# Performance work log

Measured on AMD Instinct MI355X. Metric: run time of the kernel, lower is better.

The kernel has to match this reference:

```python
import jax, jax.numpy as jnp
import numpy as np

TAU = 0.1
EPS = 1e-8

def _l2norm(x, axis):
    # matches F.normalize: x / max(||x||, 1e-12)
    n = jnp.sqrt(jnp.sum(x * x, axis=axis, keepdims=True))
    return x / jnp.maximum(n, 1e-12)

def setup_inputs() -> dict:
    key = jax.random.key(0)
    k1, k2, k3 = jax.random.split(key, 3)
    B, D, K = 262144, 256, 64
    return {
        "features": jax.random.normal(k1, (B, D), dtype=jnp.float32),
        "prototypes": jax.random.normal(k2, (K, D), dtype=jnp.float32),
        "domain_labels": jax.random.randint(k3, (B,), 0, K, dtype=jnp.int64),
    }

def reference(features, prototypes, domain_labels):
    f = _l2norm(features, 1)            # (B, D)
    p = _l2norm(prototypes, 1)          # (K, D)
    sim = jnp.einsum('bd,kd->bk', f, p) / TAU   # (B, K)
    e = jnp.exp(sim)                    # (B, K)
    numerator = jnp.take_along_axis(e, domain_labels[:, None], axis=1)[:, 0]  # (B,)
    denominator = jnp.sum(e, axis=1)    # (B,)
    loss = -jnp.log((numerator + EPS) / (denominator + EPS) + EPS)
    return jnp.mean(loss)
```

## Files before the change

kernel.cpp:

```cpp
#include <hip/hip_runtime.h>
#include <stdint.h>

typedef __attribute__((ext_vector_type(8))) short short8;
typedef __attribute__((ext_vector_type(4))) float floatx4;

#define EPS 1e-8f
#define TAU 0.1f
#define LROW 264

__device__ __forceinline__ unsigned short f2bf(float f) {
  union { float f; unsigned u; } v; v.f = f;
  unsigned u = v.u;
  u += 0x7fffu + ((u >> 16) & 1u);
  return (unsigned short)(u >> 16);
}

__device__ __forceinline__ unsigned pack2_trunc(float lo, float hi) {
  union { float f; unsigned u; } a, b; a.f = lo; b.f = hi;
  return __builtin_amdgcn_perm(b.u, a.u, 0x07060302u);
}

__device__ __forceinline__ void async_copy16(const void* g, void* l) {
  __builtin_amdgcn_global_load_lds(
      (__attribute__((address_space(1))) void*)g,
      (__attribute__((address_space(3))) void*)l, 16, 0, 0);
}

__global__ void proto_prep(const float* __restrict__ protos,
                           unsigned short* __restrict__ pbf) {
  const int l = threadIdx.x & 63;
  const int w = threadIdx.x >> 6;
  const int row = blockIdx.x * 4 + w;
  float4 v = reinterpret_cast<const float4*>(protos)[row * 64 + l];
  float ss = v.x * v.x + v.y * v.y + v.z * v.z + v.w * v.w;
#pragma unroll
  for (int d = 1; d < 64; d <<= 1) ss += __shfl_xor(ss, d, 64);
  const float inv = 1.0f / fmaxf(sqrtf(ss), 1e-12f);
  ushort4 o;
  o.x = f2bf(v.x * inv); o.y = f2bf(v.y * inv);
  o.z = f2bf(v.z * inv); o.w = f2bf(v.w * inv);
  reinterpret_cast<ushort4*>(pbf)[row * 64 + l] = o;
}

__global__ __launch_bounds__(256, 4)
void protonce_main(const float* __restrict__ feat,
                   const unsigned short* __restrict__ pbf,
                   const int* __restrict__ labels,
                   float* __restrict__ partials) {
  __shared__ __align__(16) float At[32 * LROW];
  __shared__ float dn_sm[2][32];
  __shared__ float nm_sm[2][32];

  const int tid = threadIdx.x;
  const int l = tid & 63;
  const int w = tid >> 6;
  const int mw = w & 1;
  const int nw = w >> 1;
  const int n = l & 15;
  const int q = l >> 4;
  const long rowBase = (long)blockIdx.x * 32;

  const float* srcw = feat + (rowBase + w * 8) * 256 + l * 4;
#pragma unroll
  for (int j = 0; j < 8; ++j)
    async_copy16(srcw + j * 256, &At[(w * 8 + j) * LROW]);

  const unsigned short* bbase = pbf + (nw * 32 + n) * 256 + q * 8;
  short8 bv[16];
#pragma unroll
  for (int s = 0; s < 8; ++s) {
    bv[2 * s]     = *reinterpret_cast<const short8*>(bbase + s * 32);
    bv[2 * s + 1] = *reinterpret_cast<const short8*>(bbase + 16 * 256 + s * 32);
  }

  __syncthreads();

  floatx4 acc0 = {0.f, 0.f, 0.f, 0.f}, acc1 = {0.f, 0.f, 0.f, 0.f};
  float ss = 0.f;
  const float* arow = &At[(mw * 16 + n) * LROW + q * 8];
#pragma unroll
  for (int s = 0; s < 8; ++s) {
    float4 x = *reinterpret_cast<const float4*>(arow + s * 32);
    float4 y = *reinterpret_cast<const float4*>(arow + s * 32 + 4);
    ss += x.x * x.x + x.y * x.y + x.z * x.z + x.w * x.w +
          y.x * y.x + y.y * y.y + y.z * y.z + y.w * y.w;
    union { short8 s8; uint4 u4; } af;
    af.u4.x = pack2_trunc(x.x, x.y);
    af.u4.y = pack2_trunc(x.z, x.w);
    af.u4.z = pack2_trunc(y.x, y.y);
    af.u4.w = pack2_trunc(y.z, y.w);
    acc0 = __builtin_amdgcn_mfma_f32_16x16x32_bf16(af.s8, bv[2 * s],     acc0, 0, 0, 0);
    acc1 = __builtin_amdgcn_mfma_f32_16x16x32_bf16(af.s8, bv[2 * s + 1], acc1, 0, 0, 0);
  }
  ss += __shfl_xor(ss, 16, 64);
  ss += __shfl_xor(ss, 32, 64);

  const int4 lv = *reinterpret_cast<const int4*>(labels + rowBase + mw * 16 + q * 4);
#pragma unroll
  for (int r = 0; r < 4; ++r) {
    const float nrm = __shfl(ss, q * 4 + r, 64);
    const float sc = 1.0f / (fmaxf(sqrtf(nrm), 1e-12f) * TAU);
    const int lab = (r == 0) ? lv.x : (r == 1) ? lv.y : (r == 2) ? lv.z : lv.w;
    const float e0 = __expf(acc0[r] * sc);
    const float e1 = __expf(acc1[r] * sc);
    float den = e0 + e1;
    float num = (nw * 32 + n == lab ? e0 : 0.f) + (nw * 32 + 16 + n == lab ? e1 : 0.f);
#pragma unroll
    for (int d = 1; d < 16; d <<= 1) {
      den += __shfl_xor(den, d, 64);
      num += __shfl_xor(num, d, 64);
    }
    if (n == 0) {
      dn_sm[nw][mw * 16 + q * 4 + r] = den;
      nm_sm[nw][mw * 16 + q * 4 + r] = num;
    }
  }
  __syncthreads();

  if (w == 0) {
    float loss = 0.f;
    if (l < 32) {
      const float den = dn_sm[0][l] + dn_sm[1][l];
      const float num = nm_sm[0][l] + nm_sm[1][l];
      loss = -__logf((num + EPS) / (den + EPS) + EPS);
    }
#pragma unroll
    for (int d = 1; d < 64; d <<= 1) loss += __shfl_xor(loss, d, 64);
    if (l == 0) partials[blockIdx.x] = loss;
  }
}

__global__ void finalize_k(const float* __restrict__ partials, int nblocks,
                           float* __restrict__ out, float invB) {
  __shared__ float red[256];
  float s = 0.f;
  for (int i = threadIdx.x; i < nblocks; i += 256) s += partials[i];
  red[threadIdx.x] = s;
  __syncthreads();
#pragma unroll
  for (int d = 128; d > 0; d >>= 1) {
    if (threadIdx.x < d) red[threadIdx.x] += red[threadIdx.x + d];
    __syncthreads();
  }
  if (threadIdx.x == 0) out[0] = red[0] * invB;
}

extern "C" void kernel_launch(void* const* d_in, const int* in_sizes, int n_in,
                              void* d_out, int out_size, void* d_ws, size_t ws_size,
                              hipStream_t stream) {
  const float* feat = (const float*)d_in[0];
  const float* protos = (const float*)d_in[1];
  const int* labels = (const int*)d_in[2];
  float* out = (float*)d_out;
  const int Bn = in_sizes[0] / 256;
  const int nblocks = Bn / 32;
  unsigned short* pbf = (unsigned short*)d_ws;
  float* partials = (float*)((char*)d_ws + 64 * 256 * sizeof(unsigned short));

  hipLaunchKernelGGL(proto_prep, dim3(16), dim3(256), 0, stream, protos, pbf);
  hipLaunchKernelGGL(protonce_main, dim3(nblocks), dim3(256), 0, stream,
                     feat, pbf, labels, partials);
  hipLaunchKernelGGL(finalize_k, dim3(1), dim3(256), 0, stream, partials,
                     nblocks, out, 1.0f / (float)Bn);
}
```

Measured before the change: 367.5 us.

## Process eight row tiles per block with double-buffered async LDS loads

```diff
diff --git a/kernel.cpp b/kernel.cpp
--- a/kernel.cpp
+++ b/kernel.cpp
@@ -6,7 +6,8 @@
 
 #define EPS 1e-8f
 #define TAU 0.1f
-#define LROW 264
+#define LROW 260
+#define TILES_PER_BLK 8
 
 __device__ __forceinline__ unsigned short f2bf(float f) {
   union { float f; unsigned u; } v; v.f = f;
@@ -42,14 +43,14 @@
   reinterpret_cast<ushort4*>(pbf)[row * 64 + l] = o;
 }
 
-__global__ __launch_bounds__(256, 4)
+__global__ __launch_bounds__(256, 2)
 void protonce_main(const float* __restrict__ feat,
                    const unsigned short* __restrict__ pbf,
                    const int* __restrict__ labels,
                    float* __restrict__ partials) {
-  __shared__ __align__(16) float At[32 * LROW];
-  __shared__ float dn_sm[2][32];
-  __shared__ float nm_sm[2][32];
+  __shared__ __align__(16) float Abuf[2][32 * LROW];
+  __shared__ float dn_sm[2][2][32];
+  __shared__ float nm_sm[2][2][32];
 
   const int tid = threadIdx.x;
   const int l = tid & 63;
@@ -58,12 +59,7 @@
   const int nw = w >> 1;
   const int n = l & 15;
   const int q = l >> 4;
-  const long rowBase = (long)blockIdx.x * 32;
-
-  const float* srcw = feat + (rowBase + w * 8) * 256 + l * 4;
-#pragma unroll
-  for (int j = 0; j < 8; ++j)
-    async_copy16(srcw + j * 256, &At[(w * 8 + j) * LROW]);
+  const long blockRow0 = (long)blockIdx.x * 256;
 
   const unsigned short* bbase = pbf + (nw * 32 + n) * 256 + q * 8;
   short8 bv[16];
@@ -72,61 +68,91 @@
     bv[2 * s]     = *reinterpret_cast<const short8*>(bbase + s * 32);
     bv[2 * s + 1] = *reinterpret_cast<const short8*>(bbase + 16 * 256 + s * 32);
   }
+  int4 lab[TILES_PER_BLK];
+#pragma unroll
+  for (int t = 0; t < TILES_PER_BLK; ++t)
+    lab[t] = *reinterpret_cast<const int4*>(
+        labels + blockRow0 + t * 32 + mw * 16 + q * 4);
+
+  const float* srcw = feat + (blockRow0 + w * 8) * 256 + l * 4;
+#pragma unroll
+  for (int j = 0; j < 8; ++j)
+    async_copy16(srcw + j * 256, &Abuf[0][(w * 8 + j) * LROW]);
+
+  float lossAcc = 0.f;
+
+  for (int t = 0; t < TILES_PER_BLK; ++t) {
+    const int p = t & 1;
+    __syncthreads();
+
+    if (t + 1 < TILES_PER_BLK) {
+      const float* s2 = srcw + (long)(t + 1) * 32 * 256;
+#pragma unroll
+      for (int j = 0; j < 8; ++j)
+        async_copy16(s2 + j * 256, &Abuf[p ^ 1][(w * 8 + j) * LROW]);
+    }
+
+    if (t > 0 && w == 0 && l < 32) {
+      const int pp = (t - 1) & 1;
+      const float den = dn_sm[pp][0][l] + dn_sm[pp][1][l];
+      const float num = nm_sm[pp][0][l] + nm_sm[pp][1][l];
+      lossAcc += -__logf((num + EPS) / (den + EPS) + EPS);
+    }
+
+    floatx4 acc0 = {0.f, 0.f, 0.f, 0.f}, acc1 = {0.f, 0.f, 0.f, 0.f};
+    float ss = 0.f;
+    const float* arow = &Abuf[p][(mw * 16 + n) * LROW + q * 8];
+#pragma unroll
+    for (int s = 0; s < 8; ++s) {
+      float4 x = *reinterpret_cast<const float4*>(arow + s * 32);
+      float4 y = *reinterpret_cast<const float4*>(arow + s * 32 + 4);
+      ss += x.x * x.x + x.y * x.y + x.z * x.z + x.w * x.w +
+            y.x * y.x + y.y * y.y + y.z * y.z + y.w * y.w;
+      union { short8 s8; uint4 u4; } af;
+      af.u4.x = pack2_trunc(x.x, x.y);
+      af.u4.y = pack2_trunc(x.z, x.w);
+      af.u4.z = pack2_trunc(y.x, y.y);
+      af.u4.w = pack2_trunc(y.z, y.w);
+      acc0 = __builtin_amdgcn_mfma_f32_16x16x32_bf16(af.s8, bv[2 * s],     acc0, 0, 0, 0);
+      acc1 = __builtin_amdgcn_mfma_f32_16x16x32_bf16(af.s8, bv[2 * s + 1], acc1, 0, 0, 0);
+    }
+    ss += __shfl_xor(ss, 16, 64);
+    ss += __shfl_xor(ss, 32, 64);
+
+    const int4 lv = lab[t];
+#pragma unroll
+    for (int r = 0; r < 4; ++r) {
+      const float nrm = __shfl(ss, q * 4 + r, 64);
+      const float sc = 1.0f / (fmaxf(sqrtf(nrm), 1e-12f) * TAU);
+      const int labv = (r == 0) ? lv.x : (r == 1) ? lv.y : (r == 2) ? lv.z : lv.w;
+      const float e0 = __expf(acc0[r] * sc);
+      const float e1 = __expf(acc1[r] * sc);
+      float den = e0 + e1;
+      float num = (nw * 32 + n == labv ? e0 : 0.f) +
+                  (nw * 32 + 16 + n == labv ? e1 : 0.f);
+#pragma unroll
+      for (int d = 1; d < 16; d <<= 1) {
+        den += __shfl_xor(den, d, 64);
+        num += __shfl_xor(num, d, 64);
+      }
+      if (n == 0) {
+        dn_sm[p][nw][mw * 16 + q * 4 + r] = den;
+        nm_sm[p][nw][mw * 16 + q * 4 + r] = num;
+      }
+    }
+  }
 
   __syncthreads();
-
-  floatx4 acc0 = {0.f, 0.f, 0.f, 0.f}, acc1 = {0.f, 0.f, 0.f, 0.f};
-  float ss = 0.f;
-  const float* arow = &At[(mw * 16 + n) * LROW + q * 8];
-#pragma unroll
-  for (int s = 0; s < 8; ++s) {
-    float4 x = *reinterpret_cast<const float4*>(arow + s * 32);
-    float4 y = *reinterpret_cast<const float4*>(arow + s * 32 + 4);
-    ss += x.x * x.x + x.y * x.y + x.z * x.z + x.w * x.w +
-          y.x * y.x + y.y * y.y + y.z * y.z + y.w * y.w;
-    union { short8 s8; uint4 u4; } af;
-    af.u4.x = pack2_trunc(x.x, x.y);
-    af.u4.y = pack2_trunc(x.z, x.w);
-    af.u4.z = pack2_trunc(y.x, y.y);
-    af.u4.w = pack2_trunc(y.z, y.w);
-    acc0 = __builtin_amdgcn_mfma_f32_16x16x32_bf16(af.s8, bv[2 * s],     acc0, 0, 0, 0);
-    acc1 = __builtin_amdgcn_mfma_f32_16x16x32_bf16(af.s8, bv[2 * s + 1], acc1, 0, 0, 0);
-  }
-  ss += __shfl_xor(ss, 16, 64);
-  ss += __shfl_xor(ss, 32, 64);
-
-  const int4 lv = *reinterpret_cast<const int4*>(labels + rowBase + mw * 16 + q * 4);
-#pragma unroll
-  for (int r = 0; r < 4; ++r) {
-    const float nrm = __shfl(ss, q * 4 + r, 64);
-    const float sc = 1.0f / (fmaxf(sqrtf(nrm), 1e-12f) * TAU);
-    const int lab = (r == 0) ? lv.x : (r == 1) ? lv.y : (r == 2) ? lv.z : lv.w;
-    const float e0 = __expf(acc0[r] * sc);
-    const float e1 = __expf(acc1[r] * sc);
-    float den = e0 + e1;
-    float num = (nw * 32 + n == lab ? e0 : 0.f) + (nw * 32 + 16 + n == lab ? e1 : 0.f);
-#pragma unroll
-    for (int d = 1; d < 16; d <<= 1) {
-      den += __shfl_xor(den, d, 64);
-      num += __shfl_xor(num, d, 64);
-    }
-    if (n == 0) {
-      dn_sm[nw][mw * 16 + q * 4 + r] = den;
-      nm_sm[nw][mw * 16 + q * 4 + r] = num;
-    }
-  }
-  __syncthreads();
-
   if (w == 0) {
-    float loss = 0.f;
     if (l < 32) {
-      const float den = dn_sm[0][l] + dn_sm[1][l];
-      const float num = nm_sm[0][l] + nm_sm[1][l];
-      loss = -__logf((num + EPS) / (den + EPS) + EPS);
+      const int pp = (TILES_PER_BLK - 1) & 1;
+      const float den = dn_sm[pp][0][l] + dn_sm[pp][1][l];
+      const float num = nm_sm[pp][0][l] + nm_sm[pp][1][l];
+      lossAcc += -__logf((num + EPS) / (den + EPS) + EPS);
     }
 #pragma unroll
-    for (int d = 1; d < 64; d <<= 1) loss += __shfl_xor(loss, d, 64);
-    if (l == 0) partials[blockIdx.x] = loss;
+    for (int d = 1; d < 64; d <<= 1) lossAcc += __shfl_xor(lossAcc, d, 64);
+    if (l == 0) partials[blockIdx.x] = lossAcc;
   }
 }
 
@@ -153,7 +179,7 @@
   const int* labels = (const int*)d_in[2];
   float* out = (float*)d_out;
   const int Bn = in_sizes[0] / 256;
-  const int nblocks = Bn / 32;
+  const int nblocks = Bn / 256;
   unsigned short* pbf = (unsigned short*)d_ws;
   float* partials = (float*)((char*)d_ws + 64 * 256 * sizeof(unsigned short));
 
```

Measured after the change: 374.4 us. Within noise of the previous version (+1.9%).
